# Performance work log

Hardware: AMD Instinct MI355X
Metric: run time of the kernel (lower is better)

Reference implementation:

```python
import jax, jax.numpy as jnp
import numpy as np

B, S, D = 2, 2048, 1024
H = 16
HD = D // H  # head_dim = 64


def _xavier(key, shape):
    fan_out, fan_in = shape
    bound = jnp.sqrt(6.0 / (fan_in + fan_out))
    return jax.random.uniform(key, shape, jnp.float32, -bound, bound)


def setup_inputs() -> dict:
    key = jax.random.key(0)
    kx, kqkv, ko = jax.random.split(key, 3)
    x = jax.random.normal(kx, (B, S, D), jnp.float32)
    # torch nn.Linear stores weight as [out, in]; we keep that layout and use x @ W.T
    W_qkv = _xavier(kqkv, (3 * D, D))
    b_qkv = jnp.zeros((3 * D,), jnp.float32)
    W_o = _xavier(ko, (D, D))
    b_o = jnp.zeros((D,), jnp.float32)
    return {"x": x, "W_qkv": W_qkv, "b_qkv": b_qkv, "W_o": W_o, "b_o": b_o}


def reference(x, W_qkv, b_qkv, W_o, b_o):
    b, s, d = x.shape
    h, hd = H, HD
    # qkv projection: [b, s, 3d]
    qkv = jnp.einsum("bsd,ed->bse", x, W_qkv) + b_qkv
    # [b, s, h, 3*hd] -> [b, h, s, 3*hd]
    qkv = qkv.reshape(b, s, h, 3 * hd).transpose(0, 2, 1, 3)
    q, k, v = jnp.split(qkv, 3, axis=-1)
    scale = 1.0 / jnp.sqrt(jnp.asarray(hd, x.dtype))
    logits = jnp.einsum("bhqd,bhkd->bhqk", q, k) * scale
    attn = jax.nn.softmax(logits, axis=-1)
    values = jnp.einsum("bhqk,bhkd->bhqd", attn, v)
    values = values.transpose(0, 2, 1, 3).reshape(b, s, d)
    return jnp.einsum("bsd,ed->bse", values, W_o) + b_o
```

## Files before the change

### kernel.cpp

```cpp
#include <hip/hip_runtime.h>

typedef unsigned short u16;
typedef __attribute__((ext_vector_type(8))) short bf16x8;
typedef __attribute__((ext_vector_type(4))) float f32x4;
typedef __attribute__((ext_vector_type(16))) float f32x16;
typedef __attribute__((ext_vector_type(4))) unsigned short u16x4;

__device__ __forceinline__ u16 f2bf(float f) {
    unsigned u = __float_as_uint(f);
    u = u + 0x7FFFu + ((u >> 16) & 1u);
    return (u16)(u >> 16);
}

__device__ __forceinline__ void gload16(const void* g, void* l) {
    __builtin_amdgcn_global_load_lds(
        (const __attribute__((address_space(1))) unsigned int*)g,
        (__attribute__((address_space(3))) unsigned int*)l,
        16, 0, 0);
}

__device__ __forceinline__ f32x4 mfma16(bf16x8 a, bf16x8 b, f32x4 c) {
    return __builtin_amdgcn_mfma_f32_16x16x32_bf16(a, b, c, 0, 0, 0);
}
__device__ __forceinline__ f32x16 mfma32(bf16x8 a, bf16x8 b, f32x16 c) {
    return __builtin_amdgcn_mfma_f32_32x32x16_bf16(a, b, c, 0, 0, 0);
}

__global__ __launch_bounds__(256) void cvt_all(const float* __restrict__ x,
                                               const float* __restrict__ wqkv,
                                               const float* __restrict__ wo,
                                               u16* __restrict__ dst) {
    int i = blockIdx.x * 256 + threadIdx.x;
    float4 v;
    if (i < 1048576)       v = ((const float4*)x)[i];
    else if (i < 1835008)  v = ((const float4*)wqkv)[i - 1048576];
    else                   v = ((const float4*)wo)[i - 1835008];
    u16x4 o = { f2bf(v.x), f2bf(v.y), f2bf(v.z), f2bf(v.w) };
    ((u16x4*)dst)[i] = o;
}

template <int BM, int BN, bool OUT_BF16>
__global__ __launch_bounds__(256) void gemm_bt(const u16* __restrict__ A,
                                               const u16* __restrict__ Bm,
                                               const float* __restrict__ bias,
                                               void* __restrict__ Cp,
                                               int M, int N, int K) {
    constexpr int FM = BM / 32, FN = BN / 32;
    __shared__ u16 As[BM * 64];
    __shared__ u16 Bs[BN * 64];
    const int tid = threadIdx.x, lane = tid & 63, wave = tid >> 6;
    const int wr = wave >> 1, wc = wave & 1;
    const int l15 = lane & 15, l4 = lane >> 4;

    const int nx = gridDim.x, nwg = nx * gridDim.y;
    const int id = blockIdx.y * nx + blockIdx.x;
    const int wg = (id & 7) * (nwg >> 3) + (id >> 3);
    const int m0 = (wg / nx) * BM, n0 = (wg % nx) * BN;

    f32x4 zero = {0.f, 0.f, 0.f, 0.f};
    f32x4 acc[FM][FN];
#pragma unroll
    for (int m = 0; m < FM; ++m)
#pragma unroll
        for (int n = 0; n < FN; ++n) acc[m][n] = zero;

    const int nt = K >> 6;
    for (int t = 0; t < nt; ++t) {
#pragma unroll
        for (int i = 0; i < BM / 32; ++i) {
            int c = i * 256 + tid;
            int r = c >> 3, kc = (c & 7) ^ (r & 7);
            gload16(A + (size_t)(m0 + r) * K + t * 64 + kc * 8,
                    As + (i * 256 + wave * 64) * 8);
        }
#pragma unroll
        for (int i = 0; i < BN / 32; ++i) {
            int c = i * 256 + tid;
            int r = c >> 3, kc = (c & 7) ^ (r & 7);
            gload16(Bm + (size_t)(n0 + r) * K + t * 64 + kc * 8,
                    Bs + (i * 256 + wave * 64) * 8);
        }
        __syncthreads();
#pragma unroll
        for (int kk = 0; kk < 2; ++kk) {
            bf16x8 af[FM], bfr[FN];
#pragma unroll
            for (int m = 0; m < FM; ++m) {
                int row = wr * (BM / 2) + m * 16 + l15;
                int ch = (kk * 4 + l4) ^ (row & 7);
                af[m] = *(const bf16x8*)((const char*)As + row * 128 + ch * 16);
            }
#pragma unroll
            for (int n = 0; n < FN; ++n) {
                int row = wc * (BN / 2) + n * 16 + l15;
                int ch = (kk * 4 + l4) ^ (row & 7);
                bfr[n] = *(const bf16x8*)((const char*)Bs + row * 128 + ch * 16);
            }
#pragma unroll
            for (int m = 0; m < FM; ++m)
#pragma unroll
                for (int n = 0; n < FN; ++n)
                    acc[m][n] = mfma16(af[m], bfr[n], acc[m][n]);
        }
        __syncthreads();
    }
    float bv[FN];
#pragma unroll
    for (int n = 0; n < FN; ++n) bv[n] = bias[n0 + wc * (BN / 2) + n * 16 + l15];
#pragma unroll
    for (int m = 0; m < FM; ++m) {
#pragma unroll
        for (int j = 0; j < 4; ++j) {
            size_t row = (size_t)(m0 + wr * (BM / 2) + m * 16 + l4 * 4 + j);
#pragma unroll
            for (int n = 0; n < FN; ++n) {
                int col = n0 + wc * (BN / 2) + n * 16 + l15;
                float v = acc[m][n][j] + bv[n];
                if (OUT_BF16)
                    ((u16*)Cp)[row * (size_t)N + col] = f2bf(v);
                else
                    ((float*)Cp)[row * (size_t)N + col] = v;
            }
        }
    }
}

__global__ __launch_bounds__(512) void gemm256(const u16* __restrict__ A,
                                               const u16* __restrict__ Bm,
                                               const float* __restrict__ bias,
                                               u16* __restrict__ Cp,
                                               int M, int N, int K) {
    __shared__ __align__(16) char lds[131072];
    const int tid = threadIdx.x, lane = tid & 63, wave = tid >> 6;
    const int wr = wave >> 2, wc = wave & 3;
    const int l15 = lane & 15, l4 = lane >> 4;

    const int nx = gridDim.x, nwg = nx * gridDim.y;
    const int id = blockIdx.y * nx + blockIdx.x;
    const int wg = (id & 7) * (nwg >> 3) + (id >> 3);
    const int m0 = (wg / nx) * 256, n0 = (wg % nx) * 256;

    const u16* asrc[2][2];
    const u16* bsrc[2][2];
#pragma unroll
    for (int q = 0; q < 2; ++q)
#pragma unroll
        for (int r = 0; r < 2; ++r) {
            int c = r * 512 + tid;
            int lr = c >> 3;
            int kc = (c & 7) ^ (lr & 7);
            asrc[q][r] = A  + (size_t)(m0 + lr + (lr & 64) + q * 64) * K + kc * 8;
            bsrc[q][r] = Bm + (size_t)(n0 + lr + (lr & 96) + q * 32) * K + kc * 8;
        }
    const int sd0 = wave * 1024;
    const int sd1 = 8192 + wave * 1024;

    const int roA = (wr * 64 + l15) * 128;
    const int roB = (wc * 32 + l15) * 128;
    int ch16[2];
#pragma unroll
    for (int kk = 0; kk < 2; ++kk) ch16[kk] = ((kk * 4 + l4) ^ (l15 & 7)) * 16;

    f32x4 zero = {0.f, 0.f, 0.f, 0.f};
    f32x4 acc[2][2][4][2];
#pragma unroll
    for (int a = 0; a < 2; ++a)
#pragma unroll
        for (int b = 0; b < 2; ++b)
#pragma unroll
            for (int c = 0; c < 4; ++c)
#pragma unroll
                for (int d = 0; d < 2; ++d) acc[a][b][c][d] = zero;

#define STG_A(q, tt) { char* rb = lds + (((tt) & 1) * 32768) + (q) * 16384;          \
        gload16(asrc[q][0] + (size_t)(tt) * 64, rb + sd0);                            \
        gload16(asrc[q][1] + (size_t)(tt) * 64, rb + sd1); }
#define STG_B(q, tt) { char* rb = lds + 65536 + (((tt) & 1) * 32768) + (q) * 16384;  \
        gload16(bsrc[q][0] + (size_t)(tt) * 64, rb + sd0);                            \
        gload16(bsrc[q][1] + (size_t)(tt) * 64, rb + sd1); }
#define MFMA_PH(MH, NH) {                                                             \
        __builtin_amdgcn_s_setprio(1);                                                \
        _Pragma("unroll")                                                             \
        for (int fm = 0; fm < 4; ++fm)                                                \
            _Pragma("unroll")                                                         \
            for (int fn = 0; fn < 2; ++fn)                                            \
                _Pragma("unroll")                                                     \
                for (int kk = 0; kk < 2; ++kk)                                        \
                    acc[MH][NH][fm][fn] =                                             \
                        mfma16(af[fm][kk], bfr[NH][fn][kk], acc[MH][NH][fm][fn]);     \
        __builtin_amdgcn_s_setprio(0); }

    STG_A(0, 0); STG_B(0, 0); STG_A(1, 0); STG_B(1, 0);
    asm volatile("s_waitcnt vmcnt(4)" ::: "memory");
    asm volatile("s_barrier" ::: "memory");

    bf16x8 af[4][2], bfr[2][2][2];
    const int nt = K >> 6;
    for (int t = 0; t < nt; ++t) {
        const char* Ab = lds + (t & 1) * 32768;
        const char* Bb = lds + 65536 + (t & 1) * 32768;
#pragma unroll
        for (int fm = 0; fm < 4; ++fm)
#pragma unroll
            for (int kk = 0; kk < 2; ++kk)
                af[fm][kk] = *(const bf16x8*)(Ab + roA + fm * 2048 + ch16[kk]);
#pragma unroll
        for (int fn = 0; fn < 2; ++fn)
#pragma unroll
            for (int kk = 0; kk < 2; ++kk)
                bfr[0][fn][kk] = *(const bf16x8*)(Bb + roB + fn * 2048 + ch16[kk]);
        if (t < nt - 1) STG_A(0, t + 1);
        asm volatile("s_barrier" ::: "memory");
        MFMA_PH(0, 0);
        asm volatile("s_barrier" ::: "memory");
#pragma unroll
        for (int fn = 0; fn < 2; ++fn)
#pragma unroll
            for (int kk = 0; kk < 2; ++kk)
                bfr[1][fn][kk] = *(const bf16x8*)(Bb + 16384 + roB + fn * 2048 + ch16[kk]);
        if (t < nt - 1) STG_B(0, t + 1);
        asm volatile("s_barrier" ::: "memory");
        MFMA_PH(0, 1);
        if (t < nt - 1) asm volatile("s_waitcnt vmcnt(4)" ::: "memory");
        else            asm volatile("s_waitcnt vmcnt(0)" ::: "memory");
        asm volatile("s_barrier" ::: "memory");
#pragma unroll
        for (int fm = 0; fm < 4; ++fm)
#pragma unroll
            for (int kk = 0; kk < 2; ++kk)
                af[fm][kk] = *(const bf16x8*)(Ab + 16384 + roA + fm * 2048 + ch16[kk]);
        if (t < nt - 1) STG_A(1, t + 1);
        asm volatile("s_barrier" ::: "memory");
        MFMA_PH(1, 0);
        asm volatile("s_barrier" ::: "memory");
        if (t < nt - 1) STG_B(1, t + 1);
        asm volatile("s_barrier" ::: "memory");
        MFMA_PH(1, 1);
        if (t < nt - 1) asm volatile("s_waitcnt vmcnt(4)" ::: "memory");
        asm volatile("s_barrier" ::: "memory");
    }
#undef STG_A
#undef STG_B
#undef MFMA_PH

    float bv[2][2];
#pragma unroll
    for (int nh = 0; nh < 2; ++nh)
#pragma unroll
        for (int fn = 0; fn < 2; ++fn)
            bv[nh][fn] = bias[n0 + wc * 64 + nh * 32 + fn * 16 + l15];
#pragma unroll
    for (int mh = 0; mh < 2; ++mh)
#pragma unroll
        for (int fm = 0; fm < 4; ++fm)
#pragma unroll
            for (int j = 0; j < 4; ++j) {
                size_t row = (size_t)(m0 + wr * 128 + mh * 64 + fm * 16 + l4 * 4 + j);
#pragma unroll
                for (int nh = 0; nh < 2; ++nh)
#pragma unroll
                    for (int fn = 0; fn < 2; ++fn) {
                        int col = n0 + wc * 64 + nh * 32 + fn * 16 + l15;
                        Cp[row * (size_t)N + col] =
                            f2bf(acc[mh][nh][fm][fn][j] + bv[nh][fn]);
                    }
            }
}

__global__ __launch_bounds__(256) void transpose_v(const u16* __restrict__ qkv,
                                                   u16* __restrict__ Vt) {
    __shared__ u16 tle[64][65];
    const int s0 = blockIdx.x * 64, h = blockIdx.y, b = blockIdx.z;
    const int tid = threadIdx.x;
#pragma unroll
    for (int i = 0; i < 16; ++i) {
        int idx = i * 256 + tid;
        int sk = idx >> 6, d = idx & 63;
        tle[sk][d] = qkv[(size_t)(b * 2048 + s0 + sk) * 3072 + h * 192 + 128 + d];
    }
    __syncthreads();
#pragma unroll
    for (int i = 0; i < 16; ++i) {
        int idx = i * 256 + tid;
        int d = idx >> 6, sk = idx & 63;
        Vt[((size_t)(b * 16 + h) * 64 + d) * 2048 + s0 + sk] = tle[sk][d];
    }
}

__global__ __launch_bounds__(512, 4) void attn_kernel(const u16* __restrict__ qkv,
                                                      const u16* __restrict__ Vt,
                                                      u16* __restrict__ vals) {
    __shared__ __align__(16) char lds[65536];
    const int qt = blockIdx.x, h = blockIdx.y, b = blockIdx.z;
    const int tid = threadIdx.x, lane = tid & 63, wave = tid >> 6;
    const int gtid = tid & 255, qsub = wave & 3, kvh = wave >> 2;
    const int l31 = lane & 31, hi = lane >> 5;
    const float S2E = 0.18033688f;

    const u16* qbase = qkv + (size_t)(b * 2048 + qt * 128 + qsub * 32 + l31) * 3072 + h * 192;
    bf16x8 Qf[4];
#pragma unroll
    for (int ks = 0; ks < 4; ++ks) {
        bf16x8 q = *(const bf16x8*)(qbase + ks * 16 + hi * 8);
#pragma unroll
        for (int j = 0; j < 8; ++j) {
            float f = __uint_as_float(((unsigned)(u16)q[j]) << 16) * S2E;
            q[j] = (short)f2bf(f);
        }
        Qf[ks] = q;
    }

    bf16x8 ones;
#pragma unroll
    for (int j = 0; j < 8; ++j) ones[j] = (short)0x3F80;

    const u16* kp[2];
    const u16* vp[2];
    int dst[2];
#pragma unroll
    for (int i = 0; i < 2; ++i) {
        int c = i * 256 + gtid;
        int fi = c >> 6, dl = c & 63;
        int mm = fi >> 2, ks = fi & 3;
        int row = mm * 32 + (dl & 31);
        int col = ks * 16 + (dl >> 5) * 8;
        kp[i] = qkv + (size_t)(b * 2048 + kvh * 1024 + row) * 3072 + h * 192 + 64 + col;
        vp[i] = Vt + ((size_t)((b * 16 + h) * 64 + row)) * 2048 + kvh * 1024 + col;
        dst[i] = fi * 512;
    }
    u16* Kst = (u16*)lds + kvh * 8192;
    u16* Vst = (u16*)lds + 16384 + kvh * 8192;

    f32x16 accO[2], accL;
#pragma unroll
    for (int md = 0; md < 2; ++md)
#pragma unroll
        for (int r = 0; r < 16; ++r) accO[md][r] = 0.f;
#pragma unroll
    for (int r = 0; r < 16; ++r) accL[r] = 0.f;

    const char* KsL = (const char*)Kst + lane * 16;
    const char* VsL = (const char*)Vst + lane * 16;

#pragma unroll
    for (int i = 0; i < 2; ++i) gload16(kp[i], Kst + dst[i]);
#pragma unroll
    for (int i = 0; i < 2; ++i) gload16(vp[i], Vst + dst[i]);
#pragma unroll
    for (int i = 0; i < 2; ++i) { kp[i] += 64 * 3072; vp[i] += 64; }

    for (int t = 0; t < 16; ++t) {
        if (t < 15) {
            u16* kd = Kst + ((t + 1) & 1) * 4096;
            u16* vd = Vst + ((t + 1) & 1) * 4096;
#pragma unroll
            for (int i = 0; i < 2; ++i) gload16(kp[i], kd + dst[i]);
#pragma unroll
            for (int i = 0; i < 2; ++i) gload16(vp[i], vd + dst[i]);
#pragma unroll
            for (int i = 0; i < 2; ++i) { kp[i] += 64 * 3072; vp[i] += 64; }
            asm volatile("s_waitcnt vmcnt(4)" ::: "memory");
        } else {
            asm volatile("s_waitcnt vmcnt(0)" ::: "memory");
        }
        asm volatile("s_barrier" ::: "memory");

        const char* Kb = KsL + (t & 1) * 8192;
        const char* Vb = VsL + (t & 1) * 8192;

        f32x16 sc[2];
        __builtin_amdgcn_s_setprio(1);
#pragma unroll
        for (int m = 0; m < 2; ++m) {
            f32x16 c;
#pragma unroll
            for (int r = 0; r < 16; ++r) c[r] = 0.f;
#pragma unroll
            for (int ks = 0; ks < 4; ++ks) {
                bf16x8 kf = *(const bf16x8*)(Kb + (m * 4 + ks) * 1024);
                c = mfma32(kf, Qf[ks], c);
            }
            sc[m] = c;
        }
        __builtin_amdgcn_s_setprio(0);

        bf16x8 Pf[4];
#pragma unroll
        for (int r = 0; r < 16; ++r)
            sc[0][r] = __builtin_amdgcn_exp2f(sc[0][r]);
        {
            unsigned W0[4], W1[4];
#pragma unroll
            for (int g = 0; g < 4; ++g) {
                asm("v_cvt_pk_bf16_f32 %0, %1, %2"
                    : "=v"(W0[g]) : "v"(sc[0][4 * g + 0]), "v"(sc[0][4 * g + 1]));
                asm("v_cvt_pk_bf16_f32 %0, %1, %2"
                    : "=v"(W1[g]) : "v"(sc[0][4 * g + 2]), "v"(sc[0][4 * g + 3]));
            }
#pragma unroll
            for (int kpair = 0; kpair < 2; ++kpair) {
                unsigned xa = W0[2 * kpair], ya = W0[2 * kpair + 1];
                unsigned xb = W1[2 * kpair], yb = W1[2 * kpair + 1];
                asm volatile("v_permlane32_swap_b32 %0, %1" : "+v"(xa), "+v"(ya));
                asm volatile("v_permlane32_swap_b32 %0, %1" : "+v"(xb), "+v"(yb));
                union { unsigned w[4]; bf16x8 v; } u;
                u.w[0] = xa; u.w[1] = xb; u.w[2] = ya; u.w[3] = yb;
                Pf[kpair] = u.v;
            }
        }

#pragma unroll
        for (int md = 0; md < 2; ++md) {
            f32x16 c = accO[md];
#pragma unroll
            for (int ks = 0; ks < 2; ++ks) {
                bf16x8 vf = *(const bf16x8*)(Vb + (md * 4 + ks) * 1024);
                c = mfma32(vf, Pf[ks], c);
            }
            accO[md] = c;
        }
#pragma unroll
        for (int ks = 0; ks < 2; ++ks)
            accL = mfma32(ones, Pf[ks], accL);

#pragma unroll
        for (int r = 0; r < 16; ++r)
            sc[1][r] = __builtin_amdgcn_exp2f(sc[1][r]);
        {
            unsigned W0[4], W1[4];
#pragma unroll
            for (int g = 0; g < 4; ++g) {
                asm("v_cvt_pk_bf16_f32 %0, %1, %2"
                    : "=v"(W0[g]) : "v"(sc[1][4 * g + 0]), "v"(sc[1][4 * g + 1]));
                asm("v_cvt_pk_bf16_f32 %0, %1, %2"
                    : "=v"(W1[g]) : "v"(sc[1][4 * g + 2]), "v"(sc[1][4 * g + 3]));
            }
#pragma unroll
            for (int kpair = 0; kpair < 2; ++kpair) {
                unsigned xa = W0[2 * kpair], ya = W0[2 * kpair + 1];
                unsigned xb = W1[2 * kpair], yb = W1[2 * kpair + 1];
                asm volatile("v_permlane32_swap_b32 %0, %1" : "+v"(xa), "+v"(ya));
                asm volatile("v_permlane32_swap_b32 %0, %1" : "+v"(xb), "+v"(yb));
                union { unsigned w[4]; bf16x8 v; } u;
                u.w[0] = xa; u.w[1] = xb; u.w[2] = ya; u.w[3] = yb;
                Pf[2 + kpair] = u.v;
            }
        }

#pragma unroll
        for (int md = 0; md < 2; ++md) {
            f32x16 c = accO[md];
#pragma unroll
            for (int ks = 2; ks < 4; ++ks) {
                bf16x8 vf = *(const bf16x8*)(Vb + (md * 4 + ks) * 1024);
                c = mfma32(vf, Pf[ks], c);
            }
            accO[md] = c;
        }
#pragma unroll
        for (int ks = 2; ks < 4; ++ks)
            accL = mfma32(ones, Pf[ks], accL);

        asm volatile("s_barrier" ::: "memory");
    }

    float lt = accL[0];

    float* MO = (float*)lds;
    float* ML = (float*)(lds + 32768);
    __syncthreads();
    if (kvh == 1) {
#pragma unroll
        for (int md = 0; md < 2; ++md)
#pragma unroll
            for (int g = 0; g < 4; ++g) {
                f32x4 w = { accO[md][4 * g + 0], accO[md][4 * g + 1],
                            accO[md][4 * g + 2], accO[md][4 * g + 3] };
                *(f32x4*)&MO[(qsub * 64 + lane) * 32 + md * 16 + 4 * g] = w;
            }
        ML[qsub * 64 + lane] = lt;
    }
    __syncthreads();
    if (kvh == 0) {
        float inv = 1.f / (lt + ML[qsub * 64 + lane]);
        size_t rowoff = (size_t)(b * 2048 + qt * 128 + qsub * 32 + l31) * 1024 + h * 64;
#pragma unroll
        for (int md = 0; md < 2; ++md)
#pragma unroll
            for (int g = 0; g < 4; ++g) {
                f32x4 w = *(const f32x4*)&MO[(qsub * 64 + lane) * 32 + md * 16 + 4 * g];
                u16x4 o = { f2bf((accO[md][4 * g + 0] + w[0]) * inv),
                            f2bf((accO[md][4 * g + 1] + w[1]) * inv),
                            f2bf((accO[md][4 * g + 2] + w[2]) * inv),
                            f2bf((accO[md][4 * g + 3] + w[3]) * inv) };
                *(u16x4*)(vals + rowoff + md * 32 + 8 * g + 4 * hi) = o;
            }
    }
}

extern "C" void kernel_launch(void* const* d_in, const int* in_sizes, int n_in,
                              void* d_out, int out_size, void* d_ws, size_t ws_size,
                              hipStream_t stream) {
    const float* x    = (const float*)d_in[0];
    const float* Wqkv = (const float*)d_in[1];
    const float* bqkv = (const float*)d_in[2];
    const float* Wo   = (const float*)d_in[3];
    const float* bo   = (const float*)d_in[4];
    float* out = (float*)d_out;

    char* ws = (char*)d_ws;
    u16* x_bf    = (u16*)(ws);
    u16* Wqkv_bf = (u16*)(ws + 8388608);
    u16* Wo_bf   = (u16*)(ws + 14680064);
    u16* qkv_bf  = (u16*)(ws + 16777216);
    u16* Vt      = (u16*)(ws + 41943040);
    u16* vals    = (u16*)(ws + 50331648);

    cvt_all<<<8192, 256, 0, stream>>>(x, Wqkv, Wo, x_bf);

    gemm256<<<dim3(12, 16), 512, 0, stream>>>(x_bf, Wqkv_bf, bqkv, qkv_bf,
                                              4096, 3072, 1024);

    transpose_v<<<dim3(32, 16, 2), 256, 0, stream>>>(qkv_bf, Vt);

    attn_kernel<<<dim3(16, 16, 2), 512, 0, stream>>>(qkv_bf, Vt, vals);

    gemm_bt<128, 64, false><<<dim3(16, 32), 256, 0, stream>>>(vals, Wo_bf, bo,
                                                              (void*)out, 4096, 1024, 1024);
}
```

Before: 117.7 us.

## Fuse V transpose into QKV GEMM epilogue, remap attention grid, enlarge out-proj tile

```diff
diff --git a/kernel.cpp b/kernel.cpp
--- a/kernel.cpp
+++ b/kernel.cpp
@@ -129,6 +129,7 @@
                                                const u16* __restrict__ Bm,
                                                const float* __restrict__ bias,
                                                u16* __restrict__ Cp,
+                                               u16* __restrict__ Vt,
                                                int M, int N, int K) {
     __shared__ __align__(16) char lds[131072];
     const int tid = threadIdx.x, lane = tid & 63, wave = tid >> 6;
@@ -265,25 +266,41 @@
                             f2bf(acc[mh][nh][fm][fn][j] + bv[nh][fn]);
                     }
             }
-}
-
-__global__ __launch_bounds__(256) void transpose_v(const u16* __restrict__ qkv,
-                                                   u16* __restrict__ Vt) {
-    __shared__ u16 tle[64][65];
-    const int s0 = blockIdx.x * 64, h = blockIdx.y, b = blockIdx.z;
-    const int tid = threadIdx.x;
-#pragma unroll
-    for (int i = 0; i < 16; ++i) {
-        int idx = i * 256 + tid;
-        int sk = idx >> 6, d = idx & 63;
-        tle[sk][d] = qkv[(size_t)(b * 2048 + s0 + sk) * 3072 + h * 192 + 128 + d];
-    }
+
+    const int b_ = m0 >> 11, s0_ = m0 & 2047;
+    const int hmin = (n0 + 63) / 192;
+    const int nV = ((hmin + 1) * 192 + 128 < n0 + 256) ? 128 : 64;
+#pragma unroll
+    for (int nh = 0; nh < 2; ++nh)
+#pragma unroll
+        for (int fn = 0; fn < 2; ++fn) {
+            int col = n0 + wc * 64 + nh * 32 + fn * 16 + l15;
+            int hh = col / 192;
+            int dd = col - hh * 192 - 128;
+            if (dd >= 0) {
+                int vl = (hh - hmin) * 64 + dd;
+#pragma unroll
+                for (int mh = 0; mh < 2; ++mh)
+#pragma unroll
+                    for (int fm = 0; fm < 4; ++fm) {
+                        int r0 = wr * 128 + mh * 64 + fm * 16 + l4 * 4;
+                        u16x4 w = { f2bf(acc[mh][nh][fm][fn][0] + bv[nh][fn]),
+                                    f2bf(acc[mh][nh][fm][fn][1] + bv[nh][fn]),
+                                    f2bf(acc[mh][nh][fm][fn][2] + bv[nh][fn]),
+                                    f2bf(acc[mh][nh][fm][fn][3] + bv[nh][fn]) };
+                        *(u16x4*)(lds + vl * 520 + r0 * 2) = w;
+                    }
+            }
+        }
     __syncthreads();
-#pragma unroll
-    for (int i = 0; i < 16; ++i) {
-        int idx = i * 256 + tid;
-        int d = idx >> 6, sk = idx & 63;
-        Vt[((size_t)(b * 16 + h) * 64 + d) * 2048 + s0 + sk] = tle[sk][d];
+    {
+        size_t vt_base = ((size_t)(b_ * 16 + hmin) * 64) * 2048 + s0_;
+        int nchunks = nV * 64;
+        for (int c = tid; c < nchunks; c += 512) {
+            int vl = c >> 6, sl = c & 63;
+            u16x4 w = *(const u16x4*)(lds + vl * 520 + sl * 8);
+            *(u16x4*)(Vt + (size_t)vl * 2048 + vt_base + sl * 4) = w;
+        }
     }
 }
 
@@ -291,7 +308,11 @@
                                                       const u16* __restrict__ Vt,
                                                       u16* __restrict__ vals) {
     __shared__ __align__(16) char lds[65536];
-    const int qt = blockIdx.x, h = blockIdx.y, b = blockIdx.z;
+    const int L = blockIdx.x;
+    const int ord = L >> 3;
+    const int hb = (L & 7) * 4 + (ord >> 4);
+    const int qt = ord & 15;
+    const int h = hb & 15, b = hb >> 4;
     const int tid = threadIdx.x, lane = tid & 63, wave = tid >> 6;
     const int gtid = tid & 255, qsub = wave & 3, kvh = wave >> 2;
     const int l31 = lane & 31, hi = lane >> 5;
@@ -518,13 +539,11 @@
 
     cvt_all<<<8192, 256, 0, stream>>>(x, Wqkv, Wo, x_bf);
 
-    gemm256<<<dim3(12, 16), 512, 0, stream>>>(x_bf, Wqkv_bf, bqkv, qkv_bf,
+    gemm256<<<dim3(12, 16), 512, 0, stream>>>(x_bf, Wqkv_bf, bqkv, qkv_bf, Vt,
                                               4096, 3072, 1024);
 
-    transpose_v<<<dim3(32, 16, 2), 256, 0, stream>>>(qkv_bf, Vt);
-
-    attn_kernel<<<dim3(16, 16, 2), 512, 0, stream>>>(qkv_bf, Vt, vals);
-
-    gemm_bt<128, 64, false><<<dim3(16, 32), 256, 0, stream>>>(vals, Wo_bf, bo,
+    attn_kernel<<<512, 512, 0, stream>>>(qkv_bf, Vt, vals);
+
+    gemm_bt<128, 128, false><<<dim3(8, 32), 256, 0, stream>>>(vals, Wo_bf, bo,
                                                               (void*)out, 4096, 1024, 1024);
 }
```

After: 118.8 us. About the same (+1.0%).
